# Performance work log

Hardware: AMD Instinct MI355X
Metric: run time of the kernel (lower is better)

Reference implementation:

```python
import math
import jax, jax.numpy as jnp
import numpy as np

B, S, D = 2, 2048, 512
H = 8
DH = D // H  # 64
FF = 2048


def _uniform(key, shape, c):
    return jax.random.uniform(key, shape, jnp.float32, -c, c)


def setup_inputs() -> dict:
    key = jax.random.key(0)
    ks = jax.random.split(key, 16)
    x = jax.random.normal(ks[0], (B, S, D), jnp.float32)
    c_qkv = math.sqrt(6 / (D + DH))
    wq = _uniform(ks[1], (H, D, DH), c_qkv)
    wk = _uniform(ks[2], (H, D, DH), c_qkv)
    wv = _uniform(ks[3], (H, D, DH), c_qkv)
    bq = jnp.zeros((H, DH), jnp.float32)
    bk = jnp.zeros((H, DH), jnp.float32)
    bv = jnp.zeros((H, DH), jnp.float32)
    c_o = math.sqrt(6 / (H * DH + D))
    wo = _uniform(ks[4], (H * DH, D), c_o)  # stored as (in, out)
    bo = jnp.zeros((D,), jnp.float32)
    gamma1 = jnp.ones((D,), jnp.float32)
    beta1 = jnp.zeros((D,), jnp.float32)
    c_ff = math.sqrt(6 / (D + FF))
    w1 = _uniform(ks[5], (D, FF), c_ff)
    b1 = jnp.zeros((FF,), jnp.float32)
    w2 = _uniform(ks[6], (FF, D), c_ff)
    b2 = jnp.zeros((D,), jnp.float32)
    gamma2 = jnp.ones((D,), jnp.float32)
    beta2 = jnp.zeros((D,), jnp.float32)
    return dict(x=x, wq=wq, bq=bq, wk=wk, bk=bk, wv=wv, bv=bv, wo=wo, bo=bo,
                gamma1=gamma1, beta1=beta1, w1=w1, b1=b1, w2=w2, b2=b2,
                gamma2=gamma2, beta2=beta2)


def _layernorm(x, gamma, beta):
    # matches torch: (x - mean) / std(unbiased=False), no epsilon in denom
    mean = jnp.mean(x, axis=-1, keepdims=True)
    var = jnp.mean((x - mean) ** 2, axis=-1, keepdims=True)
    return gamma * (x - mean) / jnp.sqrt(var) + beta


def reference(x, wq, bq, wk, bk, wv, bv, wo, bo, gamma1, beta1, w1, b1, w2, b2, gamma2, beta2):
    # multi-head attention: all heads batched in one einsum (same math as the per-head loop)
    q = jnp.einsum('bsd,hde->bhse', x, wq) + bq[None, :, None, :]
    k = jnp.einsum('bsd,hde->bhse', x, wk) + bk[None, :, None, :]
    v = jnp.einsum('bsd,hde->bhse', x, wv) + bv[None, :, None, :]
    scores = jnp.einsum('bhse,bhte->bhst', q, k) / math.sqrt(DH)  # [B,H,S,S]
    attn = jax.nn.softmax(scores, axis=-1)
    y = jnp.einsum('bhst,bhte->bhse', attn, v)  # [B,H,S,DH]
    y = y.transpose(0, 2, 1, 3).reshape(B, S, H * DH)
    y = y @ wo + bo
    # residual + LN (dropout is identity in eval)
    y = _layernorm(y + x, gamma1, beta1)
    # feedforward
    f = jax.nn.relu(y @ w1 + b1) @ w2 + b2
    out = _layernorm(f + y, gamma2, beta2)
    return out
```

## Files before the change

kernel.cpp:

```cpp
#include <hip/hip_runtime.h>

typedef __bf16 bf16;
typedef __attribute__((ext_vector_type(8))) __bf16 bf16x8;
typedef __attribute__((ext_vector_type(4))) float f32x4;
typedef __attribute__((ext_vector_type(16))) float f32x16;

#define DEV __device__ __forceinline__

DEV f32x4 mfma16(bf16x8 a, bf16x8 b, f32x4 c) {
  return __builtin_amdgcn_mfma_f32_16x16x32_bf16(a, b, c, 0, 0, 0);
}
DEV f32x16 mfma32(bf16x8 a, bf16x8 b, f32x16 c) {
  return __builtin_amdgcn_mfma_f32_32x32x16_bf16(a, b, c, 0, 0, 0);
}
DEV void gll16(const bf16* g, bf16* l) {
  __builtin_amdgcn_global_load_lds(
      (const __attribute__((address_space(1))) void*)g,
      (__attribute__((address_space(3))) void*)l, 16, 0, 0);
}
DEV unsigned cvtpk(float a, float b) {
  unsigned r;
  asm("v_cvt_pk_bf16_f32 %0, %1, %2" : "=v"(r) : "v"(a), "v"(b));
  return r;
}
DEV void pl32swap(unsigned& x, unsigned& y) {
  asm("v_permlane32_swap_b32 %0, %1" : "+v"(x), "+v"(y));
}

__global__ __launch_bounds__(256) void prep_k(
    const float* __restrict__ x, const float* __restrict__ wq,
    const float* __restrict__ wk, const float* __restrict__ wv,
    const float* __restrict__ wo, const float* __restrict__ w1,
    const float* __restrict__ w2, const float* __restrict__ bq,
    const float* __restrict__ bk, const float* __restrict__ bv,
    bf16* __restrict__ xb, bf16* __restrict__ wqkvT, bf16* __restrict__ woT,
    bf16* __restrict__ w1T, bf16* __restrict__ w2T, float* __restrict__ cb) {
  const int blk = blockIdx.x, tid = threadIdx.x;
  if (blk < 1024) {
    int i = blk * 256 + tid;
    const float4* p = (const float4*)x + (size_t)i * 2;
    float4 a = p[0], b = p[1];
    bf16x8 o;
    o[0] = (bf16)a.x; o[1] = (bf16)a.y; o[2] = (bf16)a.z; o[3] = (bf16)a.w;
    o[4] = (bf16)b.x; o[5] = (bf16)b.y; o[6] = (bf16)b.z; o[7] = (bf16)b.w;
    ((bf16x8*)xb)[i] = o;
    return;
  }
  if (blk == 1792) {
    for (int i = tid; i < 1536; i += 256)
      cb[i] = i < 512 ? bq[i] : (i < 1024 ? bk[i - 512] : bv[i - 1024]);
    return;
  }
  __shared__ float tile[64][65];
  const int t = blk - 1024;
  const float* src;
  bf16* dst;
  int C, Rout, r0, c0;
  if (t < 192) {
    int mat = t / 64, rem = t % 64, head = rem >> 3, rt = rem & 7;
    src = (mat == 0 ? wq : mat == 1 ? wk : wv) + head * 32768;
    dst = wqkvT + (size_t)(mat * 8 + head) * 32768;
    C = 64; Rout = 512; r0 = rt * 64; c0 = 0;
  } else if (t < 256) {
    int t2 = t - 192;
    src = wo; dst = woT; C = 512; Rout = 512;
    r0 = (t2 >> 3) * 64; c0 = (t2 & 7) * 64;
  } else if (t < 512) {
    int t2 = t - 256;
    src = w1; dst = w1T; C = 2048; Rout = 512;
    r0 = (t2 >> 5) * 64; c0 = (t2 & 31) * 64;
  } else {
    int t2 = t - 512;
    src = w2; dst = w2T; C = 512; Rout = 2048;
    r0 = (t2 >> 3) * 64; c0 = (t2 & 7) * 64;
  }
#pragma unroll
  for (int j = 0; j < 4; ++j) {
    int e = j * 256 + tid;
    int r = e >> 4, c4 = e & 15;
    float4 f = *(const float4*)(src + (size_t)(r0 + r) * C + c0 + c4 * 4);
    tile[r][c4 * 4 + 0] = f.x;
    tile[r][c4 * 4 + 1] = f.y;
    tile[r][c4 * 4 + 2] = f.z;
    tile[r][c4 * 4 + 3] = f.w;
  }
  __syncthreads();
  const int co = tid >> 2, rr0 = (tid & 3) * 16;
  bf16x8 o0, o1;
#pragma unroll
  for (int k = 0; k < 8; ++k) o0[k] = (bf16)tile[rr0 + k][co];
#pragma unroll
  for (int k = 0; k < 8; ++k) o1[k] = (bf16)tile[rr0 + 8 + k][co];
  bf16* dp = dst + (size_t)(c0 + co) * Rout + r0 + rr0;
  *(bf16x8*)dp = o0;
  *(bf16x8*)(dp + 8) = o1;
}

__global__ __launch_bounds__(256) void vtrans_k(const bf16* __restrict__ qkv,
                                                bf16* __restrict__ vtb) {
  __shared__ bf16 tile[64 * 68];
  const int tid = threadIdx.x;
  const int s0 = blockIdx.x * 64;
  const int bh = blockIdx.y, b = bh >> 3, hh = bh & 7;
  const bf16* src = qkv + 1024 + hh * 64;
#pragma unroll
  for (int j = 0; j < 2; ++j) {
    int slot = j * 256 + tid;
    int r = slot >> 3, cc = slot & 7;
    *(bf16x8*)(tile + r * 68 + cc * 8) =
        *(const bf16x8*)(src + (size_t)(b * 2048 + s0 + r) * 1536 + cc * 8);
  }
  __syncthreads();
  const int w = tid >> 6, lane = tid & 63;
#pragma unroll
  for (int sb2 = 0; sb2 < 2; ++sb2) {
    int sb = w * 2 + sb2;
    bf16x8 v;
#pragma unroll
    for (int jj = 0; jj < 8; ++jj) v[jj] = tile[(sb * 8 + jj) * 68 + lane];
    *(bf16x8*)(vtb + (size_t)bh * 131072 + (size_t)lane * 2048 + s0 + sb * 8) = v;
  }
}

template <int EPI>
__global__ __launch_bounds__(256) void gemmN64(
    const bf16* __restrict__ A, const bf16* __restrict__ Bt,
    const float* __restrict__ bias, float* __restrict__ outf,
    bf16* __restrict__ outb, int M, int N, int K, int klen) {
  __shared__ bf16 As[128 * 64];
  __shared__ bf16 Bs[64 * 64];
  const int tid = threadIdx.x;
  const int w = tid >> 6, l = tid & 63;
  const int lh = l & 15, lg = l >> 4;
  const int m0 = blockIdx.x * 128, n0 = blockIdx.y * 64;
  const int k0 = blockIdx.z * klen;
  const int mb = (w & 1) * 64, nb = (w >> 1) * 32;
  f32x4 acc[4][2] = {};
  for (int kt = k0; kt < k0 + klen; kt += 64) {
    __syncthreads();
#pragma unroll
    for (int j = 0; j < 4; ++j) {
      int slot = j * 256 + tid;
      int r = slot >> 3, cc = slot & 7;
      int kk = kt + ((cc ^ (r & 7)) << 3);
      gll16(A + (size_t)(m0 + r) * K + kk, As + slot * 8);
    }
#pragma unroll
    for (int j = 0; j < 2; ++j) {
      int slot = j * 256 + tid;
      int r = slot >> 3, cc = slot & 7;
      int kk = kt + ((cc ^ (r & 7)) << 3);
      gll16(Bt + (size_t)(n0 + r) * K + kk, Bs + slot * 8);
    }
    __syncthreads();
#pragma unroll
    for (int kk = 0; kk < 2; ++kk) {
      bf16x8 af[4], bfr[2];
#pragma unroll
      for (int mi = 0; mi < 4; ++mi) {
        int r = mb + mi * 16 + lh;
        af[mi] = *(const bf16x8*)(As + r * 64 + (((kk * 4 + lg) ^ (r & 7)) << 3));
      }
#pragma unroll
      for (int ni = 0; ni < 2; ++ni) {
        int r = nb + ni * 16 + lh;
        bfr[ni] = *(const bf16x8*)(Bs + r * 64 + (((kk * 4 + lg) ^ (r & 7)) << 3));
      }
#pragma unroll
      for (int mi = 0; mi < 4; ++mi)
#pragma unroll
        for (int ni = 0; ni < 2; ++ni)
          acc[mi][ni] = mfma16(af[mi], bfr[ni], acc[mi][ni]);
    }
  }
  float* op = (EPI == 0) ? outf + (size_t)blockIdx.z * M * N : nullptr;
#pragma unroll
  for (int mi = 0; mi < 4; ++mi)
#pragma unroll
    for (int ni = 0; ni < 2; ++ni)
#pragma unroll
      for (int i = 0; i < 4; ++i) {
        int row = m0 + mb + mi * 16 + lg * 4 + i;
        int col = n0 + nb + ni * 16 + lh;
        float v = acc[mi][ni][i];
        if (EPI == 0) {
          op[(size_t)row * N + col] = v;
        } else if (EPI == 1) {
          v += bias[col];
          outb[(size_t)row * N + col] = (bf16)fmaxf(v, 0.f);
        } else {
          v += bias[col];
          outb[(size_t)row * N + col] = (bf16)(col < 512 ? v * 0.125f : v);
        }
      }
}

__global__ __launch_bounds__(512) void attn_fwd2(
    const bf16* __restrict__ qkv,
    const bf16* __restrict__ vtb,
    bf16* __restrict__ Y) {
  __shared__ __align__(16) char lds[65536];
  const int tid = threadIdx.x;
  const int w = tid >> 6, lane = tid & 63;
  const int l31 = lane & 31, h = lane >> 5;
  const int bh = blockIdx.y, b = bh >> 3, hh = bh & 7;
  const int qtile = blockIdx.x;
  const int half = w >> 2, wp = w & 3;
  const int q0 = qtile * 128 + wp * 32;
  const int tl = tid & 255, sh = tid >> 8;

  bf16x8 qf[4];
  {
    const size_t rowQ = (size_t)(b * 2048 + q0 + l31) * 1536 + hh * 64;
#pragma unroll
    for (int g = 0; g < 4; ++g)
      qf[g] = *(const bf16x8*)(qkv + rowQ + g * 16 + h * 8);
  }
  const bf16* Kp = qkv + 512 + hh * 64;
  const bf16* Vp = vtb + (size_t)bh * 131072;

  f32x16 oacc[2] = {};
  float m_run = -1e30f, l_run = 0.f;

#define KBUF(d, hf) ((bf16*)(lds + (d) * 32768 + (hf) * 16384))
#define VBUF(d, hf) ((bf16*)(lds + (d) * 32768 + (hf) * 16384 + 8192))

  auto stage = [&](int i, int d) {
    const int k0 = sh * 1024 + i * 64;
#pragma unroll
    for (int j = 0; j < 2; ++j) {
      int slot = j * 256 + tl;
      int r = slot >> 3, cc = slot & 7;
      gll16(Kp + (size_t)(b * 2048 + k0 + r) * 1536 + ((cc ^ (r & 7)) << 3),
            KBUF(d, sh) + slot * 8);
      gll16(Vp + (size_t)r * 2048 + k0 + ((cc ^ (r & 7)) << 3),
            VBUF(d, sh) + slot * 8);
    }
  };

  stage(0, 0);
  __syncthreads();
  for (int i = 0; i < 16; ++i) {
    const int d = i & 1;
    if (i < 15) stage(i + 1, d ^ 1);
    const bf16* Kt = KBUF(d, half);
    const bf16* Vt = VBUF(d, half);
    f32x16 st[2];
#pragma unroll
    for (int kt = 0; kt < 2; ++kt) {
      f32x16 z = {};
      const int r = kt * 32 + l31;
#pragma unroll
      for (int g = 0; g < 4; ++g) {
        bf16x8 kf = *(const bf16x8*)(Kt + r * 64 + (((2 * g + h) ^ (r & 7)) << 3));
        z = mfma32(kf, qf[g], z);
      }
      st[kt] = z;
    }
    float mx = -1e30f;
#pragma unroll
    for (int kt = 0; kt < 2; ++kt)
#pragma unroll
      for (int r = 0; r < 16; ++r) mx = fmaxf(mx, st[kt][r]);
    mx = fmaxf(mx, __shfl_xor(mx, 32, 64));
    const float m_new = fmaxf(m_run, mx);
    const float scl = __expf(m_run - m_new);
    m_run = m_new;
    float ps = 0.f;
#pragma unroll
    for (int kt = 0; kt < 2; ++kt)
#pragma unroll
      for (int r = 0; r < 16; ++r) {
        float e = __expf(st[kt][r] - m_new);
        st[kt][r] = e;
        ps += e;
      }
    ps += __shfl_xor(ps, 32, 64);
    l_run = l_run * scl + ps;
    oacc[0] = oacc[0] * scl;
    oacc[1] = oacc[1] * scl;
    bf16x8 pf[4];
#pragma unroll
    for (int kt = 0; kt < 2; ++kt)
#pragma unroll
      for (int g = 0; g < 2; ++g) {
        unsigned a0 = cvtpk(st[kt][8 * g + 0], st[kt][8 * g + 1]);
        unsigned a1 = cvtpk(st[kt][8 * g + 2], st[kt][8 * g + 3]);
        unsigned b0 = cvtpk(st[kt][8 * g + 4], st[kt][8 * g + 5]);
        unsigned b1 = cvtpk(st[kt][8 * g + 6], st[kt][8 * g + 7]);
        pl32swap(a0, b0);
        pl32swap(a1, b1);
        union { unsigned u[4]; bf16x8 v; } pk;
        pk.u[0] = a0; pk.u[1] = a1; pk.u[2] = b0; pk.u[3] = b1;
        pf[kt * 2 + g] = pk.v;
      }
#pragma unroll
    for (int t = 0; t < 2; ++t) {
      const int r = t * 32 + l31;
#pragma unroll
      for (int kg = 0; kg < 4; ++kg) {
        bf16x8 vf = *(const bf16x8*)(Vt + r * 64 + (((2 * kg + h) ^ (r & 7)) << 3));
        oacc[t] = mfma32(vf, pf[kg], oacc[t]);
      }
    }
    __syncthreads();
  }

  if (half == 1) {
    char* ob = lds + wp * 8192;
#pragma unroll
    for (int t = 0; t < 2; ++t)
#pragma unroll
      for (int c = 0; c < 4; ++c) {
        f32x4 v4 = {oacc[t][c * 4 + 0], oacc[t][c * 4 + 1],
                    oacc[t][c * 4 + 2], oacc[t][c * 4 + 3]};
        *(f32x4*)(ob + (t * 4 + c) * 1024 + lane * 16) = v4;
      }
    ((float2*)(lds + 32768))[wp * 64 + lane] = make_float2(m_run, l_run);
  }
  __syncthreads();
  bf16* Yt = (bf16*)(lds + 34816);
  if (half == 0) {
    float2 ml2 = ((const float2*)(lds + 32768))[wp * 64 + lane];
    const float mstar = fmaxf(m_run, ml2.x);
    const float e1 = __expf(m_run - mstar), e2 = __expf(ml2.x - mstar);
    const float lstar = l_run * e1 + ml2.y * e2;
    const float r1 = e1 / lstar, r2 = e2 / lstar;
    const char* ob = lds + wp * 8192;
#pragma unroll
    for (int t = 0; t < 2; ++t)
#pragma unroll
      for (int c = 0; c < 4; ++c) {
        f32x4 v4 = *(const f32x4*)(ob + (t * 4 + c) * 1024 + lane * 16);
#pragma unroll
        for (int j = 0; j < 4; ++j)
          oacc[t][c * 4 + j] = oacc[t][c * 4 + j] * r1 + v4[j] * r2;
      }
#pragma unroll
    for (int t = 0; t < 2; ++t)
#pragma unroll
      for (int r = 0; r < 16; ++r) {
        int dh = (r & 3) + 8 * (r >> 2) + 4 * h + 32 * t;
        Yt[(wp * 32 + l31) * 72 + dh] = (bf16)oacc[t][r];
      }
  }
  __syncthreads();
#pragma unroll
  for (int it = 0; it < 2; ++it) {
    int s = it * 512 + tid;
    int ql = s >> 3, cbk = s & 7;
    bf16x8 v = *(const bf16x8*)(Yt + ql * 72 + cbk * 8);
    *(bf16x8*)(Y + (size_t)(b * 2048 + qtile * 128 + ql) * 512 + hh * 64 + cbk * 8) = v;
  }
#undef KBUF
#undef VBUF
}

__global__ __launch_bounds__(256) void add_ln1_k(
    const float* __restrict__ P,
    const float* __restrict__ xres, const float* __restrict__ bias,
    const float* __restrict__ gamma, const float* __restrict__ beta,
    bf16* __restrict__ outb) {
  const int row = blockIdx.x, tid = threadIdx.x;
  const size_t base = (size_t)row * 512;
  const float2 p0 = ((const float2*)(P + base))[tid];
  const float2 p1 = ((const float2*)(P + 2097152 + base))[tid];
  const float2 xr = ((const float2*)(xres + base))[tid];
  const int c = tid * 2;
  float s0 = p0.x + p1.x + bias[c] + xr.x;
  float s1 = p0.y + p1.y + bias[c + 1] + xr.y;
  float sum = s0 + s1;
#pragma unroll
  for (int m = 1; m < 64; m <<= 1) sum += __shfl_xor(sum, m, 64);
  __shared__ float part[4], part2[4];
  const int w = tid >> 6, l = tid & 63;
  if (l == 0) part[w] = sum;
  __syncthreads();
  const float mean = (part[0] + part[1] + part[2] + part[3]) * (1.f / 512.f);
  const float d0 = s0 - mean, d1 = s1 - mean;
  float vs = d0 * d0 + d1 * d1;
#pragma unroll
  for (int m = 1; m < 64; m <<= 1) vs += __shfl_xor(vs, m, 64);
  if (l == 0) part2[w] = vs;
  __syncthreads();
  const float var = (part2[0] + part2[1] + part2[2] + part2[3]) * (1.f / 512.f);
  const float inv = rsqrtf(var);
  outb[base + c] = (bf16)(gamma[c] * (d0 * inv) + beta[c]);
  outb[base + c + 1] = (bf16)(gamma[c + 1] * (d1 * inv) + beta[c + 1]);
}

__global__ __launch_bounds__(256) void add_ln2_k(
    const float* __restrict__ P,
    const bf16* __restrict__ rres, const float* __restrict__ bias,
    const float* __restrict__ gamma, const float* __restrict__ beta,
    float* __restrict__ outf) {
  const int row = blockIdx.x, tid = threadIdx.x;
  const size_t base = (size_t)row * 512;
  const float2 p0 = ((const float2*)(P + base))[tid];
  const float2 p1 = ((const float2*)(P + 2097152 + base))[tid];
  const int c = tid * 2;
  float s0 = p0.x + p1.x + bias[c] + (float)rres[base + c];
  float s1 = p0.y + p1.y + bias[c + 1] + (float)rres[base + c + 1];
  float sum = s0 + s1;
#pragma unroll
  for (int m = 1; m < 64; m <<= 1) sum += __shfl_xor(sum, m, 64);
  __shared__ float part[4], part2[4];
  const int w = tid >> 6, l = tid & 63;
  if (l == 0) part[w] = sum;
  __syncthreads();
  const float mean = (part[0] + part[1] + part[2] + part[3]) * (1.f / 512.f);
  const float d0 = s0 - mean, d1 = s1 - mean;
  float vs = d0 * d0 + d1 * d1;
#pragma unroll
  for (int m = 1; m < 64; m <<= 1) vs += __shfl_xor(vs, m, 64);
  if (l == 0) part2[w] = vs;
  __syncthreads();
  const float var = (part2[0] + part2[1] + part2[2] + part2[3]) * (1.f / 512.f);
  const float inv = rsqrtf(var);
  ((float2*)(outf + base))[tid] =
      make_float2(gamma[c] * (d0 * inv) + beta[c], gamma[c + 1] * (d1 * inv) + beta[c + 1]);
}

extern "C" void kernel_launch(void* const* d_in, const int* in_sizes, int n_in,
                              void* d_out, int out_size, void* d_ws, size_t ws_size,
                              hipStream_t stream) {
  const float* x = (const float*)d_in[0];
  const float* wq = (const float*)d_in[1];
  const float* bq = (const float*)d_in[2];
  const float* wk = (const float*)d_in[3];
  const float* bk = (const float*)d_in[4];
  const float* wv = (const float*)d_in[5];
  const float* bv = (const float*)d_in[6];
  const float* wo = (const float*)d_in[7];
  const float* bo = (const float*)d_in[8];
  const float* g1 = (const float*)d_in[9];
  const float* be1 = (const float*)d_in[10];
  const float* w1 = (const float*)d_in[11];
  const float* b1 = (const float*)d_in[12];
  const float* w2 = (const float*)d_in[13];
  const float* b2 = (const float*)d_in[14];
  const float* g2 = (const float*)d_in[15];
  const float* be2 = (const float*)d_in[16];

  char* ws = (char*)d_ws;
  bf16* xb    = (bf16*)(ws + 0);
  bf16* y1b   = (bf16*)(ws + 0);
  bf16* wqkvT = (bf16*)(ws + 4194304);
  bf16* woT   = (bf16*)(ws + 5767168);
  bf16* w1T   = (bf16*)(ws + 6291456);
  bf16* w2T   = (bf16*)(ws + 8388608);
  float* cb   = (float*)(ws + 10485760);
  bf16* qkvb  = (bf16*)(ws + 10493952);
  float* t0   = (float*)(ws + 10493952);
  bf16* f1    = (bf16*)(ws + 10493952);
  bf16* vtb   = (bf16*)(ws + 23078656);
  bf16* yb    = (bf16*)(ws + 27272960);
  float* f2   = (float*)(ws + 27272960);

  prep_k<<<1793, 256, 0, stream>>>(x, wq, wk, wv, wo, w1, w2, bq, bk, bv,
                                   xb, wqkvT, woT, w1T, w2T, cb);

  gemmN64<2><<<dim3(32, 24, 1), 256, 0, stream>>>(xb, wqkvT, cb, nullptr, qkvb,
                                                  4096, 1536, 512, 512);
  vtrans_k<<<dim3(32, 16), 256, 0, stream>>>(qkvb, vtb);
  attn_fwd2<<<dim3(16, 16), 512, 0, stream>>>(qkvb, vtb, yb);
  gemmN64<0><<<dim3(32, 8, 2), 256, 0, stream>>>(yb, woT, nullptr, t0, nullptr,
                                                 4096, 512, 512, 256);
  add_ln1_k<<<4096, 256, 0, stream>>>(t0, x, bo, g1, be1, y1b);
  gemmN64<1><<<dim3(32, 32, 1), 256, 0, stream>>>(y1b, w1T, b1, nullptr, f1,
                                                  4096, 2048, 512, 512);
  gemmN64<0><<<dim3(32, 8, 2), 256, 0, stream>>>(f1, w2T, nullptr, f2, nullptr,
                                                 4096, 512, 2048, 1024);
  add_ln2_k<<<4096, 256, 0, stream>>>(f2, y1b, b2, g2, be2, (float*)d_out);
}
```

Before: 113.4 us.

## Add 128x128 tile GEMM for FFN1 and tune attention softmax reductions

Replaces the 128x64-tile GEMM used for the first feed-forward matmul with a dedicated 128x128-tile kernel that fuses bias and ReLU, halving the grid and raising operand reuse per block. In the attention kernel, wave priority is raised around the MFMA sections, and the serial max/sum reductions over scores become tree reductions to shorten dependency chains. The larger tile uses more registers and puts fewer blocks in flight (512 for 256 CUs), which risks load imbalance.

Result: no change. 115.6 us (+1.9%).

```diff
diff --git a/kernel.cpp b/kernel.cpp
--- a/kernel.cpp
+++ b/kernel.cpp
@@ -185,13 +185,66 @@
         float v = acc[mi][ni][i];
         if (EPI == 0) {
           op[(size_t)row * N + col] = v;
-        } else if (EPI == 1) {
-          v += bias[col];
-          outb[(size_t)row * N + col] = (bf16)fmaxf(v, 0.f);
         } else {
           v += bias[col];
           outb[(size_t)row * N + col] = (bf16)(col < 512 ? v * 0.125f : v);
         }
+      }
+}
+
+__global__ __launch_bounds__(256) void gemm128relu(
+    const bf16* __restrict__ A, const bf16* __restrict__ Bt,
+    const float* __restrict__ bias, bf16* __restrict__ outb,
+    int M, int N, int K) {
+  __shared__ bf16 As[128 * 64];
+  __shared__ bf16 Bs[128 * 64];
+  const int tid = threadIdx.x;
+  const int w = tid >> 6, l = tid & 63;
+  const int lh = l & 15, lg = l >> 4;
+  const int m0 = blockIdx.x * 128, n0 = blockIdx.y * 128;
+  const int mb = (w & 1) * 64, nb = (w >> 1) * 64;
+  f32x4 acc[4][4] = {};
+  for (int kt = 0; kt < K; kt += 64) {
+    __syncthreads();
+#pragma unroll
+    for (int j = 0; j < 4; ++j) {
+      int slot = j * 256 + tid;
+      int r = slot >> 3, cc = slot & 7;
+      int kk = kt + ((cc ^ (r & 7)) << 3);
+      gll16(A + (size_t)(m0 + r) * K + kk, As + slot * 8);
+      gll16(Bt + (size_t)(n0 + r) * K + kk, Bs + slot * 8);
+    }
+    __syncthreads();
+#pragma unroll
+    for (int kk = 0; kk < 2; ++kk) {
+      bf16x8 af[4], bfr[4];
+#pragma unroll
+      for (int mi = 0; mi < 4; ++mi) {
+        int r = mb + mi * 16 + lh;
+        af[mi] = *(const bf16x8*)(As + r * 64 + (((kk * 4 + lg) ^ (r & 7)) << 3));
+      }
+#pragma unroll
+      for (int ni = 0; ni < 4; ++ni) {
+        int r = nb + ni * 16 + lh;
+        bfr[ni] = *(const bf16x8*)(Bs + r * 64 + (((kk * 4 + lg) ^ (r & 7)) << 3));
+      }
+#pragma unroll
+      for (int mi = 0; mi < 4; ++mi)
+#pragma unroll
+        for (int ni = 0; ni < 4; ++ni)
+          acc[mi][ni] = mfma16(af[mi], bfr[ni], acc[mi][ni]);
+    }
+  }
+#pragma unroll
+  for (int mi = 0; mi < 4; ++mi)
+#pragma unroll
+    for (int ni = 0; ni < 4; ++ni)
+#pragma unroll
+      for (int i = 0; i < 4; ++i) {
+        int row = m0 + mb + mi * 16 + lg * 4 + i;
+        int col = n0 + nb + ni * 16 + lh;
+        float v = acc[mi][ni][i] + bias[col];
+        outb[(size_t)row * N + col] = (bf16)fmaxf(v, 0.f);
       }
 }
 
@@ -246,6 +299,7 @@
     const bf16* Kt = KBUF(d, half);
     const bf16* Vt = VBUF(d, half);
     f32x16 st[2];
+    __builtin_amdgcn_s_setprio(1);
 #pragma unroll
     for (int kt = 0; kt < 2; ++kt) {
       f32x16 z = {};
@@ -257,25 +311,30 @@
       }
       st[kt] = z;
     }
-    float mx = -1e30f;
-#pragma unroll
-    for (int kt = 0; kt < 2; ++kt)
-#pragma unroll
-      for (int r = 0; r < 16; ++r) mx = fmaxf(mx, st[kt][r]);
-    mx = fmaxf(mx, __shfl_xor(mx, 32, 64));
+    __builtin_amdgcn_s_setprio(0);
+    float tm[16];
+#pragma unroll
+    for (int r = 0; r < 16; ++r) tm[r] = fmaxf(st[0][r], st[1][r]);
+#pragma unroll
+    for (int s = 8; s > 0; s >>= 1)
+#pragma unroll
+      for (int r = 0; r < s; ++r) tm[r] = fmaxf(tm[r], tm[r + s]);
+    float mx = fmaxf(tm[0], __shfl_xor(tm[0], 32, 64));
     const float m_new = fmaxf(m_run, mx);
     const float scl = __expf(m_run - m_new);
     m_run = m_new;
-    float ps = 0.f;
 #pragma unroll
     for (int kt = 0; kt < 2; ++kt)
 #pragma unroll
-      for (int r = 0; r < 16; ++r) {
-        float e = __expf(st[kt][r] - m_new);
-        st[kt][r] = e;
-        ps += e;
-      }
-    ps += __shfl_xor(ps, 32, 64);
+      for (int r = 0; r < 16; ++r) st[kt][r] = __expf(st[kt][r] - m_new);
+    float ts[16];
+#pragma unroll
+    for (int r = 0; r < 16; ++r) ts[r] = st[0][r] + st[1][r];
+#pragma unroll
+    for (int s = 8; s > 0; s >>= 1)
+#pragma unroll
+      for (int r = 0; r < s; ++r) ts[r] += ts[r + s];
+    float ps = ts[0] + __shfl_xor(ts[0], 32, 64);
     l_run = l_run * scl + ps;
     oacc[0] = oacc[0] * scl;
     oacc[1] = oacc[1] * scl;
@@ -294,6 +353,7 @@
         pk.u[0] = a0; pk.u[1] = a1; pk.u[2] = b0; pk.u[3] = b1;
         pf[kt * 2 + g] = pk.v;
       }
+    __builtin_amdgcn_s_setprio(1);
 #pragma unroll
     for (int t = 0; t < 2; ++t) {
       const int r = t * 32 + l31;
@@ -303,6 +363,7 @@
         oacc[t] = mfma32(vf, pf[kg], oacc[t]);
       }
     }
+    __builtin_amdgcn_s_setprio(0);
     __syncthreads();
   }
 
@@ -467,8 +528,7 @@
   gemmN64<0><<<dim3(32, 8, 2), 256, 0, stream>>>(yb, woT, nullptr, t0, nullptr,
                                                  4096, 512, 512, 256);
   add_ln1_k<<<4096, 256, 0, stream>>>(t0, x, bo, g1, be1, y1b);
-  gemmN64<1><<<dim3(32, 32, 1), 256, 0, stream>>>(y1b, w1T, b1, nullptr, f1,
-                                                  4096, 2048, 512, 512);
+  gemm128relu<<<dim3(32, 16), 256, 0, stream>>>(y1b, w1T, b1, f1, 4096, 2048, 512);
   gemmN64<0><<<dim3(32, 8, 2), 256, 0, stream>>>(f1, w2T, nullptr, f2, nullptr,
                                                  4096, 512, 2048, 1024);
   add_ln2_k<<<4096, 256, 0, stream>>>(f2, y1b, b2, g2, be2, (float*)d_out);
```
